# Performance work log

Hardware: AMD Instinct MI355X
Metric: run time of the kernel (lower is better)

The kernel has to match this reference:

```python
import jax, jax.numpy as jnp
import numpy as np

D_MODEL = 1024
N_HEADS = 16
HEAD_DIM = D_MODEL // N_HEADS


def setup_inputs() -> dict:
    key = jax.random.key(0)
    ks = jax.random.split(key, 6)
    B, S = 4, 2048
    query = jax.random.normal(ks[0], (B, S, D_MODEL), dtype=jnp.float32)
    key_value = jax.random.normal(ks[1], (B, S, D_MODEL), dtype=jnp.float32)
    scale = 1.0 / np.sqrt(D_MODEL)
    Wq = jax.random.normal(ks[2], (D_MODEL, D_MODEL), dtype=jnp.float32) * scale
    Wk = jax.random.normal(ks[3], (D_MODEL, D_MODEL), dtype=jnp.float32) * scale
    Wv = jax.random.normal(ks[4], (D_MODEL, D_MODEL), dtype=jnp.float32) * scale
    Wo = jax.random.normal(ks[5], (D_MODEL, D_MODEL), dtype=jnp.float32) * scale
    return {"query": query, "key_value": key_value, "Wq": Wq, "Wk": Wk, "Wv": Wv, "Wo": Wo}


def reference(query, key_value, Wq, Wk, Wv, Wo):
    B, S, _ = query.shape
    H, Dh = N_HEADS, HEAD_DIM
    # nn.Linear (no bias): y = x @ W.T ; then split heads -> [B, H, S, Dh]
    q = (query @ Wq.T).reshape(B, S, H, Dh).transpose(0, 2, 1, 3)
    k = (key_value @ Wk.T).reshape(B, S, H, Dh).transpose(0, 2, 1, 3)
    v = (key_value @ Wv.T).reshape(B, S, H, Dh).transpose(0, 2, 1, 3)
    scale = Dh ** -0.5
    scores = jnp.einsum("bhqd,bhkd->bhqk", q, k) * scale  # [B,H,S,S]
    causal = jnp.tril(jnp.ones((S, S), dtype=bool))  # True where allowed
    scores = jnp.where(causal, scores, -jnp.inf)
    attn = jax.nn.softmax(scores, axis=-1)
    out = jnp.einsum("bhqk,bhkd->bhqd", attn, v)  # [B,H,S,Dh]
    out = out.transpose(0, 2, 1, 3).reshape(B, S, H * Dh)
    return out @ Wo.T
```

## Files before the change

kernel.cpp:

```cpp
#include <hip/hip_runtime.h>
#include <stdint.h>

typedef unsigned short u16;
typedef __attribute__((ext_vector_type(4))) unsigned short u16x4;
typedef __attribute__((ext_vector_type(8))) unsigned short u16x8;
typedef __attribute__((ext_vector_type(8))) __bf16 bf16x8;
typedef __attribute__((ext_vector_type(2))) _Float16 half2;
typedef __attribute__((ext_vector_type(8))) _Float16 half8;
typedef __attribute__((ext_vector_type(4))) float f32x4;

#define SEQ 2048
#define DM 1024
#define NH 16
#define DH 64
#define BATCH 4
#define MROWS (BATCH * SEQ)

#define SC_LOG2E 0.18033688011112042f

__device__ __forceinline__ u16 f2bf(float f) {
    uint32_t u = __builtin_bit_cast(uint32_t, f);
    u += 0x7fffu + ((u >> 16) & 1u);
    return (u16)(u >> 16);
}
__device__ __forceinline__ u16 f2h(float f) {
    return __builtin_bit_cast(u16, (_Float16)f);
}
__device__ __forceinline__ half2 pkrtz(float a, float b) {
    return __builtin_bit_cast(half2, __builtin_amdgcn_cvt_pkrtz(a, b));
}

__device__ __forceinline__ void load16_lds(const void* g, void* l) {
    __builtin_amdgcn_global_load_lds(
        (const __attribute__((address_space(1))) uint32_t*)(uintptr_t)g,
        (__attribute__((address_space(3))) uint32_t*)(uintptr_t)l,
        16, 0, 0);
}

#define N4A (MROWS * DM / 4)
#define N4W (DM * DM / 4)

__device__ __forceinline__ void cvt_one(const float* src, u16* dst, int i) {
    float4 v = ((const float4*)src)[i];
    u16x4 o;
    o[0] = f2bf(v.x); o[1] = f2bf(v.y); o[2] = f2bf(v.z); o[3] = f2bf(v.w);
    *(u16x4*)(dst + (size_t)i * 4) = o;
}

__global__ void cvt_all(const float* __restrict__ q, const float* __restrict__ kv,
                        const float* __restrict__ w0, const float* __restrict__ w1,
                        const float* __restrict__ w2, const float* __restrict__ w3,
                        u16* __restrict__ dq, u16* __restrict__ dkv,
                        u16* __restrict__ dw0, u16* __restrict__ dw1,
                        u16* __restrict__ dw2, u16* __restrict__ dw3) {
    int i = blockIdx.x * 256 + threadIdx.x;
    if (i < N4A) { cvt_one(q, dq, i); return; }
    i -= N4A;
    if (i < N4A) { cvt_one(kv, dkv, i); return; }
    i -= N4A;
    int s = i >> 18;
    int l = i & (N4W - 1);
    const float* src = s == 0 ? w0 : s == 1 ? w1 : s == 2 ? w2 : w3;
    u16* dst = s == 0 ? dw0 : s == 1 ? dw1 : s == 2 ? dw2 : dw3;
    cvt_one(src, dst, l);
}

__device__ __forceinline__ void gcore128(const u16* __restrict__ Ag,
                                         const u16* __restrict__ Bg,
                                         int m0, int n0, f32x4 (&acc)[4][4]) {
    constexpr int BUF = 128 * 64 * 2;
    constexpr int KT = DM / 64;
    __shared__ __align__(16) u16 lds[2 * BUF];
    const int t = threadIdx.x;
    const int lane = t & 63, w = t >> 6;
    const int ln = lane & 15, quad = lane >> 4;
    const int wrow = (w >> 1) * 64, wcol = (w & 1) * 64;

    auto stage = [&](int kt, int b) {
        if (kt >= KT) kt = KT - 1;
#pragma unroll
        for (int i = 0; i < 8; ++i) {
            const int u = i * 256 + t;
            const int isB = u >> 10;
            const int v = u & 1023;
            const int row = v >> 3, c = v & 7;
            const u16* base = isB ? Bg : Ag;
            const int g0 = (isB ? n0 : m0) + row;
            load16_lds(base + (size_t)g0 * DM + kt * 64 + ((c ^ (row & 7)) << 3),
                       &lds[(size_t)b * BUF + (size_t)u * 8]);
        }
    };
    auto rdA = [&](int b, int ks, int mi) -> bf16x8 {
        const int row = wrow + mi * 16 + ln;
        return __builtin_bit_cast(bf16x8, *(const u16x8*)&lds[
            (size_t)b * BUF + row * 64 + (((ks * 4 + quad) ^ (row & 7)) << 3)]);
    };
    auto rdB = [&](int b, int ks, int nj) -> bf16x8 {
        const int row = wcol + nj * 16 + ln;
        return __builtin_bit_cast(bf16x8, *(const u16x8*)&lds[
            (size_t)b * BUF + 8192 + row * 64 + (((ks * 4 + quad) ^ (row & 7)) << 3)]);
    };

    stage(0, 0);
    asm volatile("s_waitcnt vmcnt(0)" ::: "memory");
    __builtin_amdgcn_s_barrier();

    for (int kt = 0; kt < KT; ++kt) {
        const int b = kt & 1;
        stage(kt + 1, b ^ 1);
#pragma unroll
        for (int ks = 0; ks < 2; ++ks) {
            bf16x8 af[4], bf[4];
#pragma unroll
            for (int mi = 0; mi < 4; ++mi) af[mi] = rdA(b, ks, mi);
#pragma unroll
            for (int nj = 0; nj < 4; ++nj) bf[nj] = rdB(b, ks, nj);
#pragma unroll
            for (int mi = 0; mi < 4; ++mi)
#pragma unroll
                for (int nj = 0; nj < 4; ++nj)
                    acc[mi][nj] = __builtin_amdgcn_mfma_f32_16x16x32_bf16(
                        af[mi], bf[nj], acc[mi][nj], 0, 0, 0);
        }
        asm volatile("s_waitcnt vmcnt(0)" ::: "memory");
        __builtin_amdgcn_s_barrier();
    }
}

__global__ __launch_bounds__(256, 4) void qkv_gemm(const u16* __restrict__ q_bf,
                                                   const u16* __restrict__ kv_bf,
                                                   const u16* __restrict__ wq,
                                                   const u16* __restrict__ wk,
                                                   const u16* __restrict__ wv,
                                                   u16* __restrict__ Qh,
                                                   u16* __restrict__ Kh,
                                                   u16* __restrict__ Vt) {
    const int g = blockIdx.x;
    const int xcd = g & 7, l = g >> 3;
    const int mt = xcd * 8 + (l & 7);
    const int pn = l >> 3;
    const int sel = pn >> 3;
    const int m0 = mt * 128, n0 = (pn & 7) * 128;
    const u16* A = (sel == 0) ? q_bf : kv_bf;
    const u16* B = (sel == 0) ? wq : (sel == 1 ? wk : wv);

    f32x4 acc[4][4] = {};
    gcore128(A, B, m0, n0, acc);

    const int t = threadIdx.x;
    const int lane = t & 63, w = t >> 6;
    const int ln = lane & 15, quad = lane >> 4;
    const int wrow = (w >> 1) * 64, wcol = (w & 1) * 64;

    if (sel == 2) {
#pragma unroll
        for (int mi = 0; mi < 4; ++mi) {
            int rowb = m0 + wrow + mi * 16 + quad * 4;
            int bb = rowb >> 11, s = rowb & 2047;
#pragma unroll
            for (int ni = 0; ni < 4; ++ni) {
                int col = n0 + wcol + ni * 16 + ln;
                int h = col >> 6, d = col & 63;
                u16x4 o;
#pragma unroll
                for (int r = 0; r < 4; ++r) o[r] = f2h(acc[mi][ni][r]);
                *(u16x4*)(Vt + ((size_t)(bb * NH + h) * DH + d) * SEQ + s) = o;
            }
        }
    } else {
        u16* C = sel ? Kh : Qh;
        const float scale = sel ? 1.0f : SC_LOG2E;
#pragma unroll
        for (int mi = 0; mi < 4; ++mi) {
            int rowb = m0 + wrow + mi * 16 + quad * 4;
#pragma unroll
            for (int ni = 0; ni < 4; ++ni) {
                int col = n0 + wcol + ni * 16 + ln;
                int h = col >> 6, d = col & 63;
#pragma unroll
                for (int r = 0; r < 4; ++r) {
                    int row = rowb + r;
                    int bb = row >> 11, s = row & 2047;
                    C[((size_t)((bb * NH + h) * SEQ + s) << 6) + d] = f2bf(acc[mi][ni][r] * scale);
                }
            }
        }
    }
}

__global__ __launch_bounds__(256, 4) void wo_gemm(const u16* __restrict__ A,
                                                  const u16* __restrict__ B,
                                                  float* __restrict__ Cout) {
    const int g = blockIdx.x;
    const int xcd = g & 7, l = g >> 3;
    const int mt = xcd * 8 + (l & 7);
    const int nt = l >> 3;
    const int m0 = mt * 128, n0 = nt * 128;

    f32x4 acc[4][4] = {};
    gcore128(A, B, m0, n0, acc);

    const int t = threadIdx.x;
    const int lane = t & 63, w = t >> 6;
    const int ln = lane & 15, quad = lane >> 4;
    const int wrow = (w >> 1) * 64, wcol = (w & 1) * 64;

#pragma unroll
    for (int mi = 0; mi < 4; ++mi) {
        int rowb = m0 + wrow + mi * 16 + quad * 4;
#pragma unroll
        for (int ni = 0; ni < 4; ++ni) {
            int col = n0 + wcol + ni * 16 + ln;
#pragma unroll
            for (int r = 0; r < 4; ++r)
                Cout[(size_t)(rowb + r) * DM + col] = acc[mi][ni][r];
        }
    }
}

__global__ __launch_bounds__(256) void attn_kernel(const u16* __restrict__ Q,
                                                   const u16* __restrict__ K,
                                                   const u16* __restrict__ Vt,
                                                   u16* __restrict__ AO) {
    __shared__ __align__(16) u16 qs[128 * 64];
    __shared__ __align__(16) u16 ks[64 * 64];
    __shared__ __align__(16) u16 vs[80 * 64];

    const int t = threadIdx.x;
    const int lane = t & 63, w = t >> 6;
    const int ln = lane & 15, quad = lane >> 4;
    const int l3 = ln & 7;
    const int bi = blockIdx.x;
    const int bh = bi & 63;
    const int qraw = bi >> 6;
    const int qtile = (bh & 1) ? (15 - qraw) : qraw;
    const int q0 = qtile * 128;
    const int qw0 = q0 + w * 32;
    const int ktmax = 2 * qtile + 1;
    const u16* Qb = Q + (size_t)bh * SEQ * DH;
    const u16* Kb = K + (size_t)bh * SEQ * DH;
    const u16* Vb = Vt + (size_t)bh * DH * SEQ;
    const int b = bh >> 4, h = bh & 15;

    const int cb = t & 7;
    const int r0 = t >> 3;
    const int swc = ((cb ^ (r0 & 7)) << 3);
    const int sg = ((r0 & 12) << 1) | ((r0 & 16) >> 2) | (r0 & 3);

    if (t < 128) {
        int j = t >> 3;
        u16 hv = (j == 0) ? 0x3C00 : 0;
        u16x8 o = {hv, hv, hv, hv, hv, hv, hv, hv};
        *(u16x8*)&vs[((64 + j) << 6) | (((t & 7) ^ (j & 7)) << 3)] = o;
    }

    u16x8 qreg[4];
#pragma unroll
    for (int i = 0; i < 4; ++i)
        qreg[i] = *(const u16x8*)(Qb + (size_t)(q0 + r0 + i * 32) * DH + cb * 8);
    u16x8 kreg[2], vreg[2];
#pragma unroll
    for (int i = 0; i < 2; ++i) {
        kreg[i] = *(const u16x8*)(Kb + (size_t)(i * 32 + sg) * DH + cb * 8);
        vreg[i] = *(const u16x8*)(Vb + (size_t)(r0 + i * 32) * SEQ + cb * 8);
    }

    f32x4 oaccT[2][5] = {};

    for (int kt = 0; kt <= ktmax; ++kt) {
        const int kv0 = kt * 64;
        __syncthreads();
        if (kt == 0) {
#pragma unroll
            for (int i = 0; i < 4; ++i)
                *(u16x8*)&qs[((r0 + i * 32) << 6) | swc] = qreg[i];
        }
#pragma unroll
        for (int i = 0; i < 2; ++i) {
            *(u16x8*)&ks[((r0 + i * 32) << 6) | swc] = kreg[i];
            *(u16x8*)&vs[((r0 + i * 32) << 6) | swc] = vreg[i];
        }
        __syncthreads();
        if (kt < ktmax) {
            const int kvn = kv0 + 64;
#pragma unroll
            for (int i = 0; i < 2; ++i) {
                kreg[i] = *(const u16x8*)(Kb + (size_t)(kvn + i * 32 + sg) * DH + cb * 8);
                vreg[i] = *(const u16x8*)(Vb + (size_t)(r0 + i * 32) * SEQ + kvn + cb * 8);
            }
        }

        if (kv0 >= qw0 + 32) continue;

        f32x4 st[2][4] = {};
#pragma unroll
        for (int half = 0; half < 2; ++half) {
            const int swz = (((half * 4 + quad) ^ l3) << 3);
            bf16x8 qf0 = __builtin_bit_cast(bf16x8, *(const u16x8*)&qs[((w * 32 + ln) << 6) | swz]);
            bf16x8 qf1 = __builtin_bit_cast(bf16x8, *(const u16x8*)&qs[((w * 32 + 16 + ln) << 6) | swz]);
#pragma unroll
            for (int ms = 0; ms < 4; ++ms) {
                bf16x8 kf = __builtin_bit_cast(bf16x8, *(const u16x8*)&ks[((ms * 16 + ln) << 6) | swz]);
                st[0][ms] = __builtin_amdgcn_mfma_f32_16x16x32_bf16(kf, qf0, st[0][ms], 0, 0, 0);
                st[1][ms] = __builtin_amdgcn_mfma_f32_16x16x32_bf16(kf, qf1, st[1][ms], 0, 0, 0);
            }
        }

        half8 pf[2][2];
#pragma unroll
        for (int qt2 = 0; qt2 < 2; ++qt2) {
            const int qbase = qw0 + qt2 * 16;
            if (kv0 + 63 > qbase) {
                const int relq = qbase + ln - kv0 - quad * 8;
#pragma unroll
                for (int ms = 0; ms < 4; ++ms)
#pragma unroll
                    for (int r = 0; r < 4; ++r)
                        if ((ms >> 1) * 32 + (ms & 1) * 4 + r > relq)
                            st[qt2][ms][r] = -3e38f;
            }
#pragma unroll
            for (int c = 0; c < 2; ++c) {
                half2 p0 = pkrtz(__builtin_amdgcn_exp2f(st[qt2][2 * c][0]),
                                 __builtin_amdgcn_exp2f(st[qt2][2 * c][1]));
                half2 p1 = pkrtz(__builtin_amdgcn_exp2f(st[qt2][2 * c][2]),
                                 __builtin_amdgcn_exp2f(st[qt2][2 * c][3]));
                half2 p2 = pkrtz(__builtin_amdgcn_exp2f(st[qt2][2 * c + 1][0]),
                                 __builtin_amdgcn_exp2f(st[qt2][2 * c + 1][1]));
                half2 p3 = pkrtz(__builtin_amdgcn_exp2f(st[qt2][2 * c + 1][2]),
                                 __builtin_amdgcn_exp2f(st[qt2][2 * c + 1][3]));
                half8 v;
                v[0] = p0[0]; v[1] = p0[1]; v[2] = p1[0]; v[3] = p1[1];
                v[4] = p2[0]; v[5] = p2[1]; v[6] = p3[0]; v[7] = p3[1];
                pf[qt2][c] = v;
            }
        }

#pragma unroll
        for (int c = 0; c < 2; ++c) {
            const int off = (((c * 4 + quad) ^ l3) << 3);
#pragma unroll
            for (int nd = 0; nd < 5; ++nd) {
                half8 vf = __builtin_bit_cast(half8, *(const u16x8*)&vs[((nd * 16 + ln) << 6) | off]);
                oaccT[0][nd] = __builtin_amdgcn_mfma_f32_16x16x32_f16(vf, pf[0][c], oaccT[0][nd], 0, 0, 0);
                oaccT[1][nd] = __builtin_amdgcn_mfma_f32_16x16x32_f16(vf, pf[1][c], oaccT[1][nd], 0, 0, 0);
            }
        }
    }

#pragma unroll
    for (int qt2 = 0; qt2 < 2; ++qt2) {
        float lv = __shfl(oaccT[qt2][4][0], ln, 64);
        float linv = 1.0f / lv;
        int q = q0 + w * 32 + qt2 * 16 + ln;
        size_t base = ((size_t)(b * SEQ + q) * DM) + h * DH + quad * 4;
#pragma unroll
        for (int nd = 0; nd < 4; ++nd) {
            u16x4 o;
#pragma unroll
            for (int r = 0; r < 4; ++r) o[r] = f2bf(oaccT[qt2][nd][r] * linv);
            *(u16x4*)&AO[base + nd * 16] = o;
        }
    }
}

extern "C" void kernel_launch(void* const* d_in, const int* in_sizes, int n_in,
                              void* d_out, int out_size, void* d_ws, size_t ws_size,
                              hipStream_t stream) {
    const float* query = (const float*)d_in[0];
    const float* key_value = (const float*)d_in[1];
    const float* Wq = (const float*)d_in[2];
    const float* Wk = (const float*)d_in[3];
    const float* Wv = (const float*)d_in[4];
    const float* Wo = (const float*)d_in[5];
    float* out = (float*)d_out;

    char* ws = (char*)d_ws;
    const size_t SZ_ACT = (size_t)MROWS * DM * 2;
    const size_t SZ_W = (size_t)DM * DM * 2;
    u16* q_bf  = (u16*)(ws + 0);
    u16* kv_bf = (u16*)(ws + SZ_ACT);
    u16* wq_bf = (u16*)(ws + 2 * SZ_ACT);
    u16* wk_bf = (u16*)(ws + 2 * SZ_ACT + SZ_W);
    u16* wv_bf = (u16*)(ws + 2 * SZ_ACT + 2 * SZ_W);
    u16* wo_bf = (u16*)(ws + 2 * SZ_ACT + 3 * SZ_W);
    u16* Qh    = (u16*)(ws + 2 * SZ_ACT + 4 * SZ_W);
    u16* Kh    = (u16*)(ws + 2 * SZ_ACT + 4 * SZ_W + SZ_ACT);
    u16* Vt    = (u16*)(ws + 2 * SZ_ACT + 4 * SZ_W + 2 * SZ_ACT);
    u16* AOb   = q_bf;

    const int n4_total = 2 * N4A + 4 * N4W;
    cvt_all<<<n4_total / 256, 256, 0, stream>>>(query, key_value, Wq, Wk, Wv, Wo,
                                                q_bf, kv_bf, wq_bf, wk_bf, wv_bf, wo_bf);

    qkv_gemm<<<1536, 256, 0, stream>>>(q_bf, kv_bf, wq_bf, wk_bf, wv_bf,
                                       Qh, Kh, Vt);

    attn_kernel<<<1024, 256, 0, stream>>>(Qh, Kh, Vt, AOb);

    wo_gemm<<<512, 256, 0, stream>>>(AOb, wo_bf, out);
}
```

Measured before the change: 255.8 us.

## Shrink GEMM K-tile to 32 and prefetch two stages ahead

The shared GEMM core now stages K-slices of 32 instead of 64, which halves LDS per buffer (32KB total instead of 64KB). It issues global-to-LDS loads two iterations ahead, waiting on vmcnt(4) so one stage can stay in flight while the current one is computed. Fragments are read into registers and the barrier is placed before the MFMAs, so the next stage can overwrite the same buffer while the MFMAs run at raised wave priority. The aim is better overlap of memory with compute and room for higher occupancy, at the cost of twice as many loop iterations and barriers.

```diff
diff --git a/kernel.cpp b/kernel.cpp
--- a/kernel.cpp
+++ b/kernel.cpp
@@ -15,6 +15,7 @@
 #define DH 64
 #define BATCH 4
 #define MROWS (BATCH * SEQ)
+#define KT32 (DM / 32)
 
 #define SC_LOG2E 0.18033688011112042f
 
@@ -65,64 +66,64 @@
     cvt_one(src, dst, l);
 }
 
-__device__ __forceinline__ void gcore128(const u16* __restrict__ Ag,
-                                         const u16* __restrict__ Bg,
-                                         int m0, int n0, f32x4 (&acc)[4][4]) {
-    constexpr int BUF = 128 * 64 * 2;
-    constexpr int KT = DM / 64;
-    __shared__ __align__(16) u16 lds[2 * BUF];
+__device__ __forceinline__ void gcore(const u16* __restrict__ Ag,
+                                      const u16* __restrict__ Bg,
+                                      int m0, int n0, f32x4 (&acc)[4][4]) {
+    __shared__ __align__(16) u16 lds[2 * 8192];
     const int t = threadIdx.x;
     const int lane = t & 63, w = t >> 6;
     const int ln = lane & 15, quad = lane >> 4;
     const int wrow = (w >> 1) * 64, wcol = (w & 1) * 64;
 
     auto stage = [&](int kt, int b) {
-        if (kt >= KT) kt = KT - 1;
-#pragma unroll
-        for (int i = 0; i < 8; ++i) {
+#pragma unroll
+        for (int i = 0; i < 4; ++i) {
             const int u = i * 256 + t;
-            const int isB = u >> 10;
-            const int v = u & 1023;
-            const int row = v >> 3, c = v & 7;
+            const int isB = u >> 9;
+            const int row = (u & 511) >> 2, c = u & 3;
             const u16* base = isB ? Bg : Ag;
             const int g0 = (isB ? n0 : m0) + row;
-            load16_lds(base + (size_t)g0 * DM + kt * 64 + ((c ^ (row & 7)) << 3),
-                       &lds[(size_t)b * BUF + (size_t)u * 8]);
+            load16_lds(base + (size_t)g0 * DM + kt * 32 + ((c ^ ((row >> 1) & 3)) << 3),
+                       &lds[b * 8192 + u * 8]);
         }
     };
-    auto rdA = [&](int b, int ks, int mi) -> bf16x8 {
+    auto rdA = [&](int b, int mi) -> bf16x8 {
         const int row = wrow + mi * 16 + ln;
         return __builtin_bit_cast(bf16x8, *(const u16x8*)&lds[
-            (size_t)b * BUF + row * 64 + (((ks * 4 + quad) ^ (row & 7)) << 3)]);
+            b * 8192 + row * 32 + ((quad ^ ((row >> 1) & 3)) << 3)]);
     };
-    auto rdB = [&](int b, int ks, int nj) -> bf16x8 {
+    auto rdB = [&](int b, int nj) -> bf16x8 {
         const int row = wcol + nj * 16 + ln;
         return __builtin_bit_cast(bf16x8, *(const u16x8*)&lds[
-            (size_t)b * BUF + 8192 + row * 64 + (((ks * 4 + quad) ^ (row & 7)) << 3)]);
+            b * 8192 + 4096 + row * 32 + ((quad ^ ((row >> 1) & 3)) << 3)]);
     };
 
     stage(0, 0);
-    asm volatile("s_waitcnt vmcnt(0)" ::: "memory");
+    stage(1, 1);
+    asm volatile("s_waitcnt vmcnt(4)" ::: "memory");
     __builtin_amdgcn_s_barrier();
 
-    for (int kt = 0; kt < KT; ++kt) {
+    for (int kt = 0; kt < KT32; ++kt) {
         const int b = kt & 1;
-        stage(kt + 1, b ^ 1);
-#pragma unroll
-        for (int ks = 0; ks < 2; ++ks) {
-            bf16x8 af[4], bf[4];
-#pragma unroll
-            for (int mi = 0; mi < 4; ++mi) af[mi] = rdA(b, ks, mi);
-#pragma unroll
-            for (int nj = 0; nj < 4; ++nj) bf[nj] = rdB(b, ks, nj);
-#pragma unroll
-            for (int mi = 0; mi < 4; ++mi)
-#pragma unroll
-                for (int nj = 0; nj < 4; ++nj)
-                    acc[mi][nj] = __builtin_amdgcn_mfma_f32_16x16x32_bf16(
-                        af[mi], bf[nj], acc[mi][nj], 0, 0, 0);
-        }
-        asm volatile("s_waitcnt vmcnt(0)" ::: "memory");
+        bf16x8 af[4], bf[4];
+#pragma unroll
+        for (int mi = 0; mi < 4; ++mi) af[mi] = rdA(b, mi);
+#pragma unroll
+        for (int nj = 0; nj < 4; ++nj) bf[nj] = rdB(b, nj);
+        asm volatile("s_waitcnt lgkmcnt(0)" ::: "memory");
+        __builtin_amdgcn_sched_barrier(0);
+        __builtin_amdgcn_s_barrier();
+        if (kt < KT32 - 2) stage(kt + 2, b);
+        __builtin_amdgcn_s_setprio(1);
+#pragma unroll
+        for (int mi = 0; mi < 4; ++mi)
+#pragma unroll
+            for (int nj = 0; nj < 4; ++nj)
+                acc[mi][nj] = __builtin_amdgcn_mfma_f32_16x16x32_bf16(
+                    af[mi], bf[nj], acc[mi][nj], 0, 0, 0);
+        __builtin_amdgcn_s_setprio(0);
+        if (kt < KT32 - 2) { asm volatile("s_waitcnt vmcnt(4)" ::: "memory"); }
+        else               { asm volatile("s_waitcnt vmcnt(0)" ::: "memory"); }
         __builtin_amdgcn_s_barrier();
     }
 }
@@ -145,7 +146,7 @@
     const u16* B = (sel == 0) ? wq : (sel == 1 ? wk : wv);
 
     f32x4 acc[4][4] = {};
-    gcore128(A, B, m0, n0, acc);
+    gcore(A, B, m0, n0, acc);
 
     const int t = threadIdx.x;
     const int lane = t & 63, w = t >> 6;
@@ -198,7 +199,7 @@
     const int m0 = mt * 128, n0 = nt * 128;
 
     f32x4 acc[4][4] = {};
-    gcore128(A, B, m0, n0, acc);
+    gcore(A, B, m0, n0, acc);
 
     const int t = threadIdx.x;
     const int lane = t & 63, w = t >> 6;
```

New measurement: 268.2 us. 1.05x slower.

## Fuse fp32-to-bf16 activation conversion into QKV GEMM A-tile loading

Applied to the files above, without the earlier changes.

The separate conversion pass over query and key_value is removed. The QKV GEMM now loads fp32 activations into registers two K-tiles ahead, converts them with packed bf16 instructions, and writes them into swizzled LDS while B tiles still arrive through direct global-to-LDS loads. The aim is to avoid writing and re-reading two bf16 activation copies (about 32MB of traffic) plus a kernel launch. It also adds s_setprio around the MFMA blocks and lowers the occupancy hint to 2 for both GEMMs. The cost is higher register pressure and more global traffic per tile, since each A tile is fetched as fp32 and read several times across N tiles.

```diff
diff --git a/kernel.cpp b/kernel.cpp
--- a/kernel.cpp
+++ b/kernel.cpp
@@ -8,6 +8,7 @@
 typedef __attribute__((ext_vector_type(2))) _Float16 half2;
 typedef __attribute__((ext_vector_type(8))) _Float16 half8;
 typedef __attribute__((ext_vector_type(4))) float f32x4;
+typedef __attribute__((ext_vector_type(4))) uint32_t u32x4;
 
 #define SEQ 2048
 #define DM 1024
@@ -15,6 +16,7 @@
 #define DH 64
 #define BATCH 4
 #define MROWS (BATCH * SEQ)
+#define KT64 (DM / 64)
 
 #define SC_LOG2E 0.18033688011112042f
 
@@ -37,7 +39,6 @@
         16, 0, 0);
 }
 
-#define N4A (MROWS * DM / 4)
 #define N4W (DM * DM / 4)
 
 __device__ __forceinline__ void cvt_one(const float* src, u16* dst, int i) {
@@ -47,29 +48,172 @@
     *(u16x4*)(dst + (size_t)i * 4) = o;
 }
 
-__global__ void cvt_all(const float* __restrict__ q, const float* __restrict__ kv,
-                        const float* __restrict__ w0, const float* __restrict__ w1,
-                        const float* __restrict__ w2, const float* __restrict__ w3,
-                        u16* __restrict__ dq, u16* __restrict__ dkv,
-                        u16* __restrict__ dw0, u16* __restrict__ dw1,
-                        u16* __restrict__ dw2, u16* __restrict__ dw3) {
+__global__ void cvt_w(const float* __restrict__ w0, const float* __restrict__ w1,
+                      const float* __restrict__ w2, const float* __restrict__ w3,
+                      u16* __restrict__ d0, u16* __restrict__ d1,
+                      u16* __restrict__ d2, u16* __restrict__ d3) {
     int i = blockIdx.x * 256 + threadIdx.x;
-    if (i < N4A) { cvt_one(q, dq, i); return; }
-    i -= N4A;
-    if (i < N4A) { cvt_one(kv, dkv, i); return; }
-    i -= N4A;
     int s = i >> 18;
     int l = i & (N4W - 1);
     const float* src = s == 0 ? w0 : s == 1 ? w1 : s == 2 ? w2 : w3;
-    u16* dst = s == 0 ? dw0 : s == 1 ? dw1 : s == 2 ? dw2 : dw3;
+    u16* dst = s == 0 ? d0 : s == 1 ? d1 : s == 2 ? d2 : d3;
     cvt_one(src, dst, l);
+}
+
+#define QBUF 16384
+
+__global__ __launch_bounds__(256, 2) void qkv_gemm(const float* __restrict__ qf,
+                                                   const float* __restrict__ kvf,
+                                                   const u16* __restrict__ wq,
+                                                   const u16* __restrict__ wk,
+                                                   const u16* __restrict__ wv,
+                                                   u16* __restrict__ Qh,
+                                                   u16* __restrict__ Kh,
+                                                   u16* __restrict__ Vt) {
+    __shared__ __align__(16) u16 lds[2 * QBUF];
+    const int g = blockIdx.x;
+    const int xcd = g & 7, l = g >> 3;
+    const int mt = xcd * 8 + (l & 7);
+    const int pn = l >> 3;
+    const int sel = pn >> 3;
+    const int m0 = mt * 128, n0 = (pn & 7) * 128;
+    const float* Af = (sel == 0) ? qf : kvf;
+    const u16* Bg = (sel == 0) ? wq : (sel == 1 ? wk : wv);
+
+    const int t = threadIdx.x;
+    const int lane = t & 63, w = t >> 6;
+    const int ln = lane & 15, quad = lane >> 4;
+    const int wrow = (w >> 1) * 64, wcol = (w & 1) * 64;
+
+    const float* Ath = Af + (size_t)(m0 + (t >> 1)) * DM + (t & 1) * 32;
+    const int arow = t >> 1;
+    const int acj0 = (t & 1) * 4;
+
+    auto stageB = [&](int kt, int b) {
+#pragma unroll
+        for (int i = 0; i < 4; ++i) {
+            const int u = i * 256 + t;
+            const int row = u >> 3, c = u & 7;
+            load16_lds(Bg + (size_t)(n0 + row) * DM + kt * 64 + ((c ^ (row & 7)) << 3),
+                       &lds[b * QBUF + 8192 + u * 8]);
+        }
+    };
+    auto loadA = [&](f32x4 (&r)[8], int kt) {
+#pragma unroll
+        for (int j = 0; j < 8; ++j)
+            r[j] = *(const f32x4*)(Ath + kt * 64 + j * 4);
+    };
+    auto cvtwrite = [&](const f32x4 (&r)[8], int b) {
+#pragma unroll
+        for (int c4 = 0; c4 < 4; ++c4) {
+            uint32_t w0, w1, w2, w3;
+            asm("v_cvt_pk_bf16_f32 %0, %1, %2" : "=v"(w0) : "v"(r[2 * c4][0]), "v"(r[2 * c4][1]));
+            asm("v_cvt_pk_bf16_f32 %0, %1, %2" : "=v"(w1) : "v"(r[2 * c4][2]), "v"(r[2 * c4][3]));
+            asm("v_cvt_pk_bf16_f32 %0, %1, %2" : "=v"(w2) : "v"(r[2 * c4 + 1][0]), "v"(r[2 * c4 + 1][1]));
+            asm("v_cvt_pk_bf16_f32 %0, %1, %2" : "=v"(w3) : "v"(r[2 * c4 + 1][2]), "v"(r[2 * c4 + 1][3]));
+            u32x4 q = {w0, w1, w2, w3};
+            const int cj = acj0 + c4;
+            *(u32x4*)&lds[b * QBUF + arow * 64 + ((cj ^ (arow & 7)) << 3)] = q;
+        }
+    };
+    auto rdA = [&](int b, int ks, int mi) -> bf16x8 {
+        const int row = wrow + mi * 16 + ln;
+        return __builtin_bit_cast(bf16x8, *(const u16x8*)&lds[
+            b * QBUF + row * 64 + (((ks * 4 + quad) ^ (row & 7)) << 3)]);
+    };
+    auto rdB = [&](int b, int ks, int nj) -> bf16x8 {
+        const int row = wcol + nj * 16 + ln;
+        return __builtin_bit_cast(bf16x8, *(const u16x8*)&lds[
+            b * QBUF + 8192 + row * 64 + (((ks * 4 + quad) ^ (row & 7)) << 3)]);
+    };
+
+    f32x4 acc[4][4] = {};
+    f32x4 rA0[8], rA1[8];
+
+    stageB(0, 0);
+    __builtin_amdgcn_sched_barrier(0);
+    {
+        f32x4 atmp[8];
+        loadA(atmp, 0);
+        loadA(rA0, 1);
+        cvtwrite(atmp, 0);
+    }
+    asm volatile("s_waitcnt lgkmcnt(0)" ::: "memory");
+    __builtin_amdgcn_s_barrier();
+
+    auto body = [&](int kt, int b, f32x4 (&rcur)[8], f32x4 (&rnext)[8]) {
+        if (kt < KT64 - 1) {
+            stageB(kt + 1, b ^ 1);
+            __builtin_amdgcn_sched_barrier(0);
+        }
+        if (kt < KT64 - 2) loadA(rnext, kt + 2);
+        if (kt < KT64 - 1) cvtwrite(rcur, b ^ 1);
+#pragma unroll
+        for (int ks = 0; ks < 2; ++ks) {
+            bf16x8 af[4], bf[4];
+#pragma unroll
+            for (int mi = 0; mi < 4; ++mi) af[mi] = rdA(b, ks, mi);
+#pragma unroll
+            for (int nj = 0; nj < 4; ++nj) bf[nj] = rdB(b, ks, nj);
+            __builtin_amdgcn_s_setprio(1);
+#pragma unroll
+            for (int mi = 0; mi < 4; ++mi)
+#pragma unroll
+                for (int nj = 0; nj < 4; ++nj)
+                    acc[mi][nj] = __builtin_amdgcn_mfma_f32_16x16x32_bf16(
+                        af[mi], bf[nj], acc[mi][nj], 0, 0, 0);
+            __builtin_amdgcn_s_setprio(0);
+        }
+        asm volatile("s_waitcnt lgkmcnt(0)" ::: "memory");
+        if (kt < KT64 - 2) { asm volatile("s_waitcnt vmcnt(8)" ::: "memory"); }
+        else               { asm volatile("s_waitcnt vmcnt(0)" ::: "memory"); }
+        __builtin_amdgcn_s_barrier();
+    };
+    for (int k2 = 0; k2 < KT64; k2 += 2) {
+        body(k2, 0, rA0, rA1);
+        body(k2 + 1, 1, rA1, rA0);
+    }
+
+    if (sel == 2) {
+#pragma unroll
+        for (int mi = 0; mi < 4; ++mi) {
+            int rowb = m0 + wrow + mi * 16 + quad * 4;
+            int bb = rowb >> 11, s = rowb & 2047;
+#pragma unroll
+            for (int ni = 0; ni < 4; ++ni) {
+                int col = n0 + wcol + ni * 16 + ln;
+                int h = col >> 6, d = col & 63;
+                u16x4 o;
+#pragma unroll
+                for (int r = 0; r < 4; ++r) o[r] = f2h(acc[mi][ni][r]);
+                *(u16x4*)(Vt + ((size_t)(bb * NH + h) * DH + d) * SEQ + s) = o;
+            }
+        }
+    } else {
+        u16* C = sel ? Kh : Qh;
+        const float scale = sel ? 1.0f : SC_LOG2E;
+#pragma unroll
+        for (int mi = 0; mi < 4; ++mi) {
+            int rowb = m0 + wrow + mi * 16 + quad * 4;
+#pragma unroll
+            for (int ni = 0; ni < 4; ++ni) {
+                int col = n0 + wcol + ni * 16 + ln;
+                int h = col >> 6, d = col & 63;
+#pragma unroll
+                for (int r = 0; r < 4; ++r) {
+                    int row = rowb + r;
+                    int bb = row >> 11, s = row & 2047;
+                    C[((size_t)((bb * NH + h) * SEQ + s) << 6) + d] = f2bf(acc[mi][ni][r] * scale);
+                }
+            }
+        }
+    }
 }
 
 __device__ __forceinline__ void gcore128(const u16* __restrict__ Ag,
                                          const u16* __restrict__ Bg,
                                          int m0, int n0, f32x4 (&acc)[4][4]) {
     constexpr int BUF = 128 * 64 * 2;
-    constexpr int KT = DM / 64;
     __shared__ __align__(16) u16 lds[2 * BUF];
     const int t = threadIdx.x;
     const int lane = t & 63, w = t >> 6;
@@ -77,7 +221,7 @@
     const int wrow = (w >> 1) * 64, wcol = (w & 1) * 64;
 
     auto stage = [&](int kt, int b) {
-        if (kt >= KT) kt = KT - 1;
+        if (kt >= KT64) kt = KT64 - 1;
 #pragma unroll
         for (int i = 0; i < 8; ++i) {
             const int u = i * 256 + t;
@@ -105,7 +249,7 @@
     asm volatile("s_waitcnt vmcnt(0)" ::: "memory");
     __builtin_amdgcn_s_barrier();
 
-    for (int kt = 0; kt < KT; ++kt) {
+    for (int kt = 0; kt < KT64; ++kt) {
         const int b = kt & 1;
         stage(kt + 1, b ^ 1);
 #pragma unroll
@@ -115,80 +259,21 @@
             for (int mi = 0; mi < 4; ++mi) af[mi] = rdA(b, ks, mi);
 #pragma unroll
             for (int nj = 0; nj < 4; ++nj) bf[nj] = rdB(b, ks, nj);
+            __builtin_amdgcn_s_setprio(1);
 #pragma unroll
             for (int mi = 0; mi < 4; ++mi)
 #pragma unroll
                 for (int nj = 0; nj < 4; ++nj)
                     acc[mi][nj] = __builtin_amdgcn_mfma_f32_16x16x32_bf16(
                         af[mi], bf[nj], acc[mi][nj], 0, 0, 0);
+            __builtin_amdgcn_s_setprio(0);
         }
         asm volatile("s_waitcnt vmcnt(0)" ::: "memory");
         __builtin_amdgcn_s_barrier();
     }
 }
 
-__global__ __launch_bounds__(256, 4) void qkv_gemm(const u16* __restrict__ q_bf,
-                                                   const u16* __restrict__ kv_bf,
-                                                   const u16* __restrict__ wq,
-                                                   const u16* __restrict__ wk,
-                                                   const u16* __restrict__ wv,
-                                                   u16* __restrict__ Qh,
-                                                   u16* __restrict__ Kh,
-                                                   u16* __restrict__ Vt) {
-    const int g = blockIdx.x;
-    const int xcd = g & 7, l = g >> 3;
-    const int mt = xcd * 8 + (l & 7);
-    const int pn = l >> 3;
-    const int sel = pn >> 3;
-    const int m0 = mt * 128, n0 = (pn & 7) * 128;
-    const u16* A = (sel == 0) ? q_bf : kv_bf;
-    const u16* B = (sel == 0) ? wq : (sel == 1 ? wk : wv);
-
-    f32x4 acc[4][4] = {};
-    gcore128(A, B, m0, n0, acc);
-
-    const int t = threadIdx.x;
-    const int lane = t & 63, w = t >> 6;
-    const int ln = lane & 15, quad = lane >> 4;
-    const int wrow = (w >> 1) * 64, wcol = (w & 1) * 64;
-
-    if (sel == 2) {
-#pragma unroll
-        for (int mi = 0; mi < 4; ++mi) {
-            int rowb = m0 + wrow + mi * 16 + quad * 4;
-            int bb = rowb >> 11, s = rowb & 2047;
-#pragma unroll
-            for (int ni = 0; ni < 4; ++ni) {
-                int col = n0 + wcol + ni * 16 + ln;
-                int h = col >> 6, d = col & 63;
-                u16x4 o;
-#pragma unroll
-                for (int r = 0; r < 4; ++r) o[r] = f2h(acc[mi][ni][r]);
-                *(u16x4*)(Vt + ((size_t)(bb * NH + h) * DH + d) * SEQ + s) = o;
-            }
-        }
-    } else {
-        u16* C = sel ? Kh : Qh;
-        const float scale = sel ? 1.0f : SC_LOG2E;
-#pragma unroll
-        for (int mi = 0; mi < 4; ++mi) {
-            int rowb = m0 + wrow + mi * 16 + quad * 4;
-#pragma unroll
-            for (int ni = 0; ni < 4; ++ni) {
-                int col = n0 + wcol + ni * 16 + ln;
-                int h = col >> 6, d = col & 63;
-#pragma unroll
-                for (int r = 0; r < 4; ++r) {
-                    int row = rowb + r;
-                    int bb = row >> 11, s = row & 2047;
-                    C[((size_t)((bb * NH + h) * SEQ + s) << 6) + d] = f2bf(acc[mi][ni][r] * scale);
-                }
-            }
-        }
-    }
-}
-
-__global__ __launch_bounds__(256, 4) void wo_gemm(const u16* __restrict__ A,
+__global__ __launch_bounds__(256, 2) void wo_gemm(const u16* __restrict__ A,
                                                   const u16* __restrict__ B,
                                                   float* __restrict__ Cout) {
     const int g = blockIdx.x;
@@ -378,8 +463,7 @@
     char* ws = (char*)d_ws;
     const size_t SZ_ACT = (size_t)MROWS * DM * 2;
     const size_t SZ_W = (size_t)DM * DM * 2;
-    u16* q_bf  = (u16*)(ws + 0);
-    u16* kv_bf = (u16*)(ws + SZ_ACT);
+    u16* AOb   = (u16*)(ws + 0);
     u16* wq_bf = (u16*)(ws + 2 * SZ_ACT);
     u16* wk_bf = (u16*)(ws + 2 * SZ_ACT + SZ_W);
     u16* wv_bf = (u16*)(ws + 2 * SZ_ACT + 2 * SZ_W);
@@ -387,13 +471,11 @@
     u16* Qh    = (u16*)(ws + 2 * SZ_ACT + 4 * SZ_W);
     u16* Kh    = (u16*)(ws + 2 * SZ_ACT + 4 * SZ_W + SZ_ACT);
     u16* Vt    = (u16*)(ws + 2 * SZ_ACT + 4 * SZ_W + 2 * SZ_ACT);
-    u16* AOb   = q_bf;
-
-    const int n4_total = 2 * N4A + 4 * N4W;
-    cvt_all<<<n4_total / 256, 256, 0, stream>>>(query, key_value, Wq, Wk, Wv, Wo,
-                                                q_bf, kv_bf, wq_bf, wk_bf, wv_bf, wo_bf);
-
-    qkv_gemm<<<1536, 256, 0, stream>>>(q_bf, kv_bf, wq_bf, wk_bf, wv_bf,
+
+    cvt_w<<<4 * N4W / 256, 256, 0, stream>>>(Wq, Wk, Wv, Wo,
+                                             wq_bf, wk_bf, wv_bf, wo_bf);
+
+    qkv_gemm<<<1536, 256, 0, stream>>>(query, key_value, wq_bf, wk_bf, wv_bf,
                                        Qh, Kh, Vt);
 
     attn_kernel<<<1024, 256, 0, stream>>>(Qh, Kh, Vt, AOb);
```

Result: slower. 305.4 us (+19.4%).

## Double-buffer K/V shared tiles and keep Q fragments in registers

Applied to the files above, without the earlier changes.

Q fragments now load straight from global memory into registers in MFMA operand layout. This drops the Q shared-memory tile and its per-tile LDS reads. K and V shared tiles become double-buffered and indexed by iteration parity, which removes one of the two __syncthreads per KV tile. LDS use stays about the same, while register pressure rises from holding the Q fragments. The per-lane Q global loads are less coalesced than before.

```diff
diff --git a/kernel.cpp b/kernel.cpp
--- a/kernel.cpp
+++ b/kernel.cpp
@@ -222,9 +222,8 @@
                                                    const u16* __restrict__ K,
                                                    const u16* __restrict__ Vt,
                                                    u16* __restrict__ AO) {
-    __shared__ __align__(16) u16 qs[128 * 64];
-    __shared__ __align__(16) u16 ks[64 * 64];
-    __shared__ __align__(16) u16 vs[80 * 64];
+    __shared__ __align__(16) u16 ks2[2][64 * 64];
+    __shared__ __align__(16) u16 vs2[2][80 * 64];
 
     const int t = threadIdx.x;
     const int lane = t & 63, w = t >> 6;
@@ -247,17 +246,22 @@
     const int swc = ((cb ^ (r0 & 7)) << 3);
     const int sg = ((r0 & 12) << 1) | ((r0 & 16) >> 2) | (r0 & 3);
 
-    if (t < 128) {
-        int j = t >> 3;
+    {
+        const int bufi = t >> 7, tt = t & 127;
+        const int j = tt >> 3;
         u16 hv = (j == 0) ? 0x3C00 : 0;
         u16x8 o = {hv, hv, hv, hv, hv, hv, hv, hv};
-        *(u16x8*)&vs[((64 + j) << 6) | (((t & 7) ^ (j & 7)) << 3)] = o;
-    }
-
-    u16x8 qreg[4];
-#pragma unroll
-    for (int i = 0; i < 4; ++i)
-        qreg[i] = *(const u16x8*)(Qb + (size_t)(q0 + r0 + i * 32) * DH + cb * 8);
+        *(u16x8*)&vs2[bufi][((64 + j) << 6) | (((tt & 7) ^ (j & 7)) << 3)] = o;
+    }
+
+    bf16x8 qh[2][2];
+#pragma unroll
+    for (int half = 0; half < 2; ++half)
+#pragma unroll
+        for (int r = 0; r < 2; ++r)
+            qh[half][r] = __builtin_bit_cast(bf16x8, *(const u16x8*)(
+                Qb + (size_t)(q0 + w * 32 + r * 16 + ln) * DH + (half * 4 + quad) * 8));
+
     u16x8 kreg[2], vreg[2];
 #pragma unroll
     for (int i = 0; i < 2; ++i) {
@@ -269,16 +273,11 @@
 
     for (int kt = 0; kt <= ktmax; ++kt) {
         const int kv0 = kt * 64;
-        __syncthreads();
-        if (kt == 0) {
-#pragma unroll
-            for (int i = 0; i < 4; ++i)
-                *(u16x8*)&qs[((r0 + i * 32) << 6) | swc] = qreg[i];
-        }
+        const int bb = kt & 1;
 #pragma unroll
         for (int i = 0; i < 2; ++i) {
-            *(u16x8*)&ks[((r0 + i * 32) << 6) | swc] = kreg[i];
-            *(u16x8*)&vs[((r0 + i * 32) << 6) | swc] = vreg[i];
+            *(u16x8*)&ks2[bb][((r0 + i * 32) << 6) | swc] = kreg[i];
+            *(u16x8*)&vs2[bb][((r0 + i * 32) << 6) | swc] = vreg[i];
         }
         __syncthreads();
         if (kt < ktmax) {
@@ -296,13 +295,11 @@
 #pragma unroll
         for (int half = 0; half < 2; ++half) {
             const int swz = (((half * 4 + quad) ^ l3) << 3);
-            bf16x8 qf0 = __builtin_bit_cast(bf16x8, *(const u16x8*)&qs[((w * 32 + ln) << 6) | swz]);
-            bf16x8 qf1 = __builtin_bit_cast(bf16x8, *(const u16x8*)&qs[((w * 32 + 16 + ln) << 6) | swz]);
 #pragma unroll
             for (int ms = 0; ms < 4; ++ms) {
-                bf16x8 kf = __builtin_bit_cast(bf16x8, *(const u16x8*)&ks[((ms * 16 + ln) << 6) | swz]);
-                st[0][ms] = __builtin_amdgcn_mfma_f32_16x16x32_bf16(kf, qf0, st[0][ms], 0, 0, 0);
-                st[1][ms] = __builtin_amdgcn_mfma_f32_16x16x32_bf16(kf, qf1, st[1][ms], 0, 0, 0);
+                bf16x8 kf = __builtin_bit_cast(bf16x8, *(const u16x8*)&ks2[bb][((ms * 16 + ln) << 6) | swz]);
+                st[0][ms] = __builtin_amdgcn_mfma_f32_16x16x32_bf16(kf, qh[half][0], st[0][ms], 0, 0, 0);
+                st[1][ms] = __builtin_amdgcn_mfma_f32_16x16x32_bf16(kf, qh[half][1], st[1][ms], 0, 0, 0);
             }
         }
 
@@ -341,7 +338,7 @@
             const int off = (((c * 4 + quad) ^ l3) << 3);
 #pragma unroll
             for (int nd = 0; nd < 5; ++nd) {
-                half8 vf = __builtin_bit_cast(half8, *(const u16x8*)&vs[((nd * 16 + ln) << 6) | off]);
+                half8 vf = __builtin_bit_cast(half8, *(const u16x8*)&vs2[bb][((nd * 16 + ln) << 6) | off]);
                 oaccT[0][nd] = __builtin_amdgcn_mfma_f32_16x16x32_f16(vf, pf[0][c], oaccT[0][nd], 0, 0, 0);
                 oaccT[1][nd] = __builtin_amdgcn_mfma_f32_16x16x32_f16(vf, pf[1][c], oaccT[1][nd], 0, 0, 0);
             }
```

Result: slower. 271.0 us (+6.0%).
